# Optimization experiments

Hardware: AMD Instinct MI355X
Metric: run time of the kernel (lower is better)

The kernel has to match this reference:

```python
import jax, jax.numpy as jnp
import numpy as np

L, H, D_IN, D_OUT = 2, 768, 768, 512


def _gru_layer(x, w_ih, w_hh, b_ih, b_hh):
    # x: [B,T,D]; w_ih: [3H,D]; w_hh: [3H,H]; b_ih,b_hh: [3H]
    # PyTorch GRU gate order: r, z, n
    gates_x = jnp.einsum('btd,gd->btg', x, w_ih) + b_ih  # [B,T,3H], precomputed once
    gates_x = jnp.swapaxes(gates_x, 0, 1)  # [T,B,3H] for scan over time
    h0 = jnp.zeros((x.shape[0], w_hh.shape[1]), dtype=x.dtype)

    def step(h, gx):
        gh = h @ w_hh.T + b_hh  # [B,3H]
        xr, xz, xn = jnp.split(gx, 3, axis=-1)
        hr, hz, hn = jnp.split(gh, 3, axis=-1)
        r = jax.nn.sigmoid(xr + hr)
        z = jax.nn.sigmoid(xz + hz)
        n = jnp.tanh(xn + r * hn)
        h_new = (1.0 - z) * n + z * h
        return h_new, h_new

    _, ys = jax.lax.scan(step, h0, gates_x)  # ys: [T,B,H]
    return jnp.swapaxes(ys, 0, 1)  # [B,T,H]


def setup_inputs() -> dict:
    key = jax.random.key(0)
    ks = jax.random.split(key, 6)
    B, T = 16, 1024
    s = 1.0 / np.sqrt(H)  # PyTorch RNN init scale
    x = jax.random.normal(ks[0], (B, T, D_IN), dtype=jnp.float32)
    # stacked per-layer GRU weights (D_IN == H so layer 0 stacks cleanly)
    w_ih = jax.random.uniform(ks[1], (L, 3 * H, H), minval=-s, maxval=s, dtype=jnp.float32)
    w_hh = jax.random.uniform(ks[2], (L, 3 * H, H), minval=-s, maxval=s, dtype=jnp.float32)
    b_ih = jax.random.uniform(ks[3], (L, 3 * H), minval=-s, maxval=s, dtype=jnp.float32)
    b_hh = jax.random.uniform(ks[4], (L, 3 * H), minval=-s, maxval=s, dtype=jnp.float32)
    w_fc = jax.random.normal(ks[5], (D_OUT, H), dtype=jnp.float32) * 0.02
    b_fc = jnp.zeros((D_OUT,), dtype=jnp.float32)
    return {"x": x, "w_ih": w_ih, "w_hh": w_hh, "b_ih": b_ih, "b_hh": b_hh,
            "w_fc": w_fc, "b_fc": b_fc}


def reference(x, w_ih, w_hh, b_ih, b_hh, w_fc, b_fc):
    out = x
    for l in range(L):  # small fixed layer loop
        out = _gru_layer(out, w_ih[l], w_hh[l], b_ih[l], b_hh[l])
    out = jnp.einsum('bth,oh->bto', out, w_fc) + b_fc  # Linear(768->512)
    return jax.nn.gelu(out, approximate=False)  # torch gelu (exact)
```

## Files before the change

### kernel.cpp

```cpp
#include <hip/hip_runtime.h>
#include <hip/hip_bf16.h>

#define H     768
#define HPAD  776
#define G3    2304
#define BATCH 16
#define TLEN  1024
#define DOUT  512
#define SLICE 32
#define WPG   24
#define NWG   96
#define NTHR  384

typedef __attribute__((ext_vector_type(8))) short short8;
typedef __attribute__((ext_vector_type(4))) float f32x4;

union U8 { short8 s; unsigned u[4]; unsigned long long q[2]; uint4 v4; };

__device__ __forceinline__ float b2f(ushort u) {
  union { unsigned int ui; float f; } v; v.ui = ((unsigned int)u) << 16; return v.f;
}
__device__ __forceinline__ ushort f2b(float f) {
  union { float f; unsigned int ui; } v; v.f = f;
  unsigned int u = v.ui;
  return (ushort)((u + 0x7fffu + ((u >> 16) & 1u)) >> 16);
}

__device__ __forceinline__ unsigned long long agent_ld64(const void* p) {
  return __hip_atomic_load((const unsigned long long*)p, __ATOMIC_RELAXED, __HIP_MEMORY_SCOPE_AGENT);
}
__device__ __forceinline__ unsigned agent_ld32(const void* p) {
  return __hip_atomic_load((const unsigned*)p, __ATOMIC_RELAXED, __HIP_MEMORY_SCOPE_AGENT);
}
__device__ __forceinline__ void agent_st32(void* p, unsigned v) {
  __hip_atomic_store((unsigned*)p, v, __ATOMIC_RELAXED, __HIP_MEMORY_SCOPE_AGENT);
}
__device__ __forceinline__ void agent_st64(void* p, unsigned long long v) {
  __hip_atomic_store((unsigned long long*)p, v, __ATOMIC_RELAXED, __HIP_MEMORY_SCOPE_AGENT);
}

__device__ __forceinline__ short8 loadA8(const void* base, bool bf, size_t eidx) {
  if (bf) return *(const short8*)((const ushort*)base + eidx);
  const uint4* f = (const uint4*)((const float*)base + eidx);
  uint4 lo = f[0];
  uint4 hi = f[1];
  U8 r;
  r.u[0] = __builtin_amdgcn_perm(lo.y, lo.x, 0x07060302);
  r.u[1] = __builtin_amdgcn_perm(lo.w, lo.z, 0x07060302);
  r.u[2] = __builtin_amdgcn_perm(hi.y, hi.x, 0x07060302);
  r.u[3] = __builtin_amdgcn_perm(hi.w, hi.z, 0x07060302);
  return r.s;
}
__device__ __forceinline__ short8 loadW8(const void* base, bool bf, size_t eidx) {
  if (bf) return *(const short8*)((const ushort*)base + eidx);
  const float* f = (const float*)base + eidx;
  short8 r;
  #pragma unroll
  for (int i = 0; i < 8; i++) r[i] = (short)f2b(f[i]);
  return r;
}
__device__ __forceinline__ float loadS(const void* p, bool bf, size_t i) {
  return bf ? b2f(((const ushort*)p)[i]) : ((const float*)p)[i];
}

__device__ __forceinline__ bool detect_bf16(const unsigned* xw, int tid, int nthr, int* sh) {
  if (tid == 0) *sh = 0;
  __syncthreads();
  int c = 0;
  for (int i = tid; i < 4096; i += nthr) {
    int e = (int)((xw[i] >> 7) & 0xFF);
    c += (e >= 110 && e <= 140) ? 1 : 0;
  }
  atomicAdd(sh, c);
  __syncthreads();
  return *sh > 2048;
}

__device__ __forceinline__ unsigned* flagp(unsigned* flags, int grp, int wgi, int rep) {
  return flags + (((grp * WPG + wgi) * 4 + rep) * 32);
}

__global__ __launch_bounds__(NTHR) void scan_kernel(
    const void* __restrict__ x,
    const void* __restrict__ w_ih,
    const void* __restrict__ w_hh,
    const void* __restrict__ b_ih,
    const void* __restrict__ b_hh,
    unsigned int* flags,
    unsigned int* dflag,
    ushort* h1buf,
    ushort* h2buf,
    float*  gxbuf1,
    float*  gxbuf2,
    ushort* y2)
{
  const int wg   = blockIdx.x;
  const int grp  = wg / WPG;
  const int wgi  = wg % WPG;
  const int tid  = threadIdx.x;
  const int wave = tid >> 6;
  const int lane = tid & 63;
  const int quad = lane >> 4;

  __shared__ ushort h_lds[BATCH * HPAD];
  __shared__ float ghs[96 * 17];
  __shared__ float hold[BATCH * SLICE];
  __shared__ float bih_s[96], bhh_s[96];
  __shared__ int   detsh;

  const bool isbf = detect_bf16((const unsigned*)x, tid, NTHR, &detsh);
  if (tid == 0) dflag[0] = isbf ? 1u : 0u;

  for (int i = tid; i < BATCH * SLICE; i += NTHR) hold[i] = 0.0f;

  if (grp == 1 || grp == 3) {
    size_t boff = (grp == 3) ? (size_t)G3 : 0;
    for (int gf = tid; gf < 96; gf += NTHR) {
      size_t gidx = boff + (size_t)(gf >> 5) * H + wgi * SLICE + (gf & 31);
      bih_s[gf] = loadS(b_ih, isbf, gidx);
      bhh_s[gf] = loadS(b_hh, isbf, gidx);
    }
  }

  const unsigned* pollp = nullptr;
  if (wave == 0) {
    if (grp == 0) {
      if (lane == 0) pollp = flagp(flags, 1, wgi, 1);
    } else if (grp == 1) {
      if      (lane == 0)  pollp = flagp(flags, 0, wgi, 1);
      else if (lane <= 24) pollp = flagp(flags, 1, lane - 1, 0);
      else if (lane <= 48) pollp = flagp(flags, 2, lane - 25, 2);
    } else if (grp == 2) {
      if      (lane < 24)  pollp = flagp(flags, 1, lane, 2);
      else if (lane == 24) pollp = flagp(flags, 3, wgi, 1);
    } else {
      if      (lane == 0)  pollp = flagp(flags, 2, wgi, 1);
      else if (lane <= 24) pollp = flagp(flags, 3, lane - 1, 0);
    }
  }

  const void* Wmat = (grp == 0 || grp == 2) ? w_ih : w_hh;
  const size_t woff = (grp >= 2) ? (size_t)G3 * H : 0;
  const int gate   = wave >> 1;
  const int gfbase = gate * SLICE + (wave & 1) * 16;
  const int nrow   = gate * H + wgi * SLICE + (wave & 1) * 16 + (lane & 15);
  const size_t wbase = woff + (size_t)nrow * H + quad * 8;

  short8 bfrag[24];
  #pragma unroll
  for (int kk = 0; kk < 24; kk++)
    bfrag[kk] = loadW8(Wmat, isbf, wbase + kk * 32);

  const int sb  = tid / 24;
  const int seg = tid % 24;

  const int pb = tid >> 4;
  const int pj = (tid & 15) * 2;
  const bool pact = (tid < BATCH * SLICE / 2);

  __syncthreads();

  for (int t = 0; t < TLEN + 3; t++) {
    if (wave == 0) {
      const unsigned tgt = (unsigned)t;
      for (;;) {
        unsigned v = pollp ? agent_ld32(pollp) : 0xFFFFFFFFu;
        if (__ballot(v < tgt) == 0ull) break;
        __builtin_amdgcn_s_sleep(1);
      }
    }
    __syncthreads();

    const int par = t & 1;
    int tau;
    if      (grp == 0) tau = t;
    else if (grp == 1) tau = t - 1;
    else if (grp == 2) tau = t - 2;
    else               tau = t - 3;
    const bool active = (tau >= 0) && (tau < TLEN);
    const bool isL = (grp == 1 || grp == 3);

    if (active) {
      const int opar = tau & 1;

      unsigned long long gr01 = 0, gz01 = 0, gn01 = 0;
      const float* gxin = nullptr;
      if (isL) {
        gxin = ((grp == 1) ? gxbuf1 : gxbuf2) + ((size_t)(opar * WPG + wgi) * BATCH) * 96;
        if (pact) {
          const float* gxr = gxin + (size_t)pb * 96;
          gr01 = agent_ld64(gxr + pj);
          gz01 = agent_ld64(gxr + 32 + pj);
          gn01 = agent_ld64(gxr + 64 + pj);
        }
      }

      if (grp == 0) {
        const size_t srcbase = ((size_t)sb * TLEN + tau) * H + seg * 32;
        #pragma unroll
        for (int i = 0; i < 4; i++) {
          short8 v = loadA8(x, isbf, srcbase + i * 8);
          *(short8*)&h_lds[sb * HPAD + seg * 32 + i * 8] = v;
        }
      } else {
        const ushort* hsrc = ((grp == 3) ? h2buf : h1buf) + (size_t)par * (BATCH * H);
        const ushort* src = hsrc + (size_t)sb * H + seg * 32;
        U8 a, b;
        a.q[0] = agent_ld64(src +  0); a.q[1] = agent_ld64(src +  4);
        b.q[0] = agent_ld64(src +  8); b.q[1] = agent_ld64(src + 12);
        U8 c, d;
        c.q[0] = agent_ld64(src + 16); c.q[1] = agent_ld64(src + 20);
        d.q[0] = agent_ld64(src + 24); d.q[1] = agent_ld64(src + 28);
        ushort* dst = &h_lds[sb * HPAD + seg * 32];
        *(uint4*)(dst + 0)  = a.v4;
        *(uint4*)(dst + 8)  = b.v4;
        *(uint4*)(dst + 16) = c.v4;
        *(uint4*)(dst + 24) = d.v4;
      }
      __syncthreads();

      const ushort* arow = &h_lds[(lane & 15) * HPAD + quad * 8];
      f32x4 acc0 = {0.f, 0.f, 0.f, 0.f}, acc1 = {0.f, 0.f, 0.f, 0.f};
      #pragma unroll
      for (int kk = 0; kk < 12; kk++) {
        short8 a0 = *(const short8*)(arow + kk * 32);
        short8 a1 = *(const short8*)(arow + (kk + 12) * 32);
        acc0 = __builtin_amdgcn_mfma_f32_16x16x32_bf16(a0, bfrag[kk],      acc0, 0, 0, 0);
        acc1 = __builtin_amdgcn_mfma_f32_16x16x32_bf16(a1, bfrag[kk + 12], acc1, 0, 0, 0);
      }
      f32x4 acc = acc0 + acc1;

      #pragma unroll
      for (int i = 0; i < 4; i++)
        ghs[(gfbase + (lane & 15)) * 17 + quad * 4 + i] = acc[i];
      __syncthreads();

      if (!isL) {
        float* gxout = ((grp == 0) ? gxbuf1 : gxbuf2) + ((size_t)(par * WPG + wgi) * BATCH) * 96;
        const int m  = tid / 24;
        const int c4 = (tid % 24) * 4;
        union { unsigned long long q; float f[2]; } p0, p1;
        p0.f[0] = ghs[(c4 + 0) * 17 + m];
        p0.f[1] = ghs[(c4 + 1) * 17 + m];
        p1.f[0] = ghs[(c4 + 2) * 17 + m];
        p1.f[1] = ghs[(c4 + 3) * 17 + m];
        agent_st64(gxout + (size_t)m * 96 + c4,     p0.q);
        agent_st64(gxout + (size_t)m * 96 + c4 + 2, p1.q);
      } else if (pact) {
        union { unsigned long long q; float f[2]; } ur, uz, un;
        ur.q = gr01; uz.q = gz01; un.q = gn01;
        ushort* hout = ((grp == 1) ? h1buf : h2buf) + (size_t)opar * (BATCH * H);
        unsigned hpack = 0;
        #pragma unroll
        for (int s = 0; s < 2; s++) {
          const int j = pj + s;
          float rpre = ur.f[s] + bih_s[j]      + ghs[j * 17 + pb]        + bhh_s[j];
          float zpre = uz.f[s] + bih_s[32 + j] + ghs[(32 + j) * 17 + pb] + bhh_s[32 + j];
          float hn   = ghs[(64 + j) * 17 + pb] + bhh_s[64 + j];
          float r = 1.0f / (1.0f + expf(-rpre));
          float z = 1.0f / (1.0f + expf(-zpre));
          float n = tanhf(un.f[s] + bih_s[64 + j] + r * hn);
          float hnew = (1.0f - z) * n + z * hold[pb * SLICE + j];
          hold[pb * SLICE + j] = hnew;
          hpack |= ((unsigned)f2b(hnew)) << (16 * s);
        }
        agent_st32(&hout[(size_t)pb * H + wgi * SLICE + pj], hpack);
        if (grp == 3)
          *(unsigned*)&y2[((size_t)pb * TLEN + tau) * H + wgi * SLICE + pj] = hpack;
      }
    }

    __syncthreads();
    if (tid < 4) agent_st32(flagp(flags, grp, wgi, tid), (unsigned)(t + 1));
  }
}

__global__ __launch_bounds__(256) void fc_kernel(
    const ushort* __restrict__ y2,
    const void* __restrict__ w_fc,
    const void* __restrict__ b_fc,
    const unsigned* __restrict__ dflag,
    void* __restrict__ out)
{
  const bool isbf = dflag[0] != 0u;
  const int wave = threadIdx.x >> 6;
  const int lane = threadIdx.x & 63;
  const int col  = lane & 15;
  const int quad = lane >> 4;
  const int m0 = blockIdx.x * 64 + wave * 16;
  const int n0 = blockIdx.y * 64;

  const ushort* arow = y2 + (size_t)(m0 + col) * H + quad * 8;
  const size_t bbase = (size_t)(n0 + col) * H + quad * 8;

  f32x4 acc[4];
  #pragma unroll
  for (int nt = 0; nt < 4; nt++) acc[nt] = (f32x4){0.f, 0.f, 0.f, 0.f};

  for (int kk = 0; kk < 24; kk++) {
    short8 a = *(const short8*)(arow + kk * 32);
    #pragma unroll
    for (int nt = 0; nt < 4; nt++) {
      short8 b = loadA8(w_fc, isbf, bbase + (size_t)nt * 16 * H + kk * 32);
      acc[nt] = __builtin_amdgcn_mfma_f32_16x16x32_bf16(a, b, acc[nt], 0, 0, 0);
    }
  }

  #pragma unroll
  for (int nt = 0; nt < 4; nt++) {
    #pragma unroll
    for (int i = 0; i < 4; i++) {
      int m = m0 + quad * 4 + i;
      int n = n0 + nt * 16 + col;
      float v = acc[nt][i] + loadS(b_fc, isbf, n);
      float g = 0.5f * v * (1.0f + erff(v * 0.70710678118654752f));
      if (isbf) ((ushort*)out)[(size_t)m * DOUT + n] = f2b(g);
      else      ((float*)out)[(size_t)m * DOUT + n] = g;
    }
  }
}

extern "C" void kernel_launch(void* const* d_in, const int* in_sizes, int n_in,
                              void* d_out, int out_size, void* d_ws, size_t ws_size,
                              hipStream_t stream) {
  const void* x    = d_in[0];
  const void* w_ih = d_in[1];
  const void* w_hh = d_in[2];
  const void* b_ih = d_in[3];
  const void* b_hh = d_in[4];
  const void* w_fc = d_in[5];
  const void* b_fc = d_in[6];

  char* ws = (char*)d_ws;
  unsigned int* flags = (unsigned int*)(ws);
  unsigned int* dflag = (unsigned int*)(ws + 49152);
  ushort* h1buf  = (ushort*)(ws + 53248);
  ushort* h2buf  = (ushort*)(ws + 102400);
  float*  gxbuf1 = (float*)(ws + 151552);
  float*  gxbuf2 = (float*)(ws + 446464);
  ushort* y2     = (ushort*)(ws + 741376);

  hipMemsetAsync(ws, 0, 151552, stream);
  scan_kernel<<<dim3(NWG), dim3(NTHR), 0, stream>>>(
      x, w_ih, w_hh, b_ih, b_hh, flags, dflag,
      h1buf, h2buf, gxbuf1, gxbuf2, y2);
  fc_kernel<<<dim3(16384 / 64, DOUT / 64), dim3(256), 0, stream>>>(
      y2, w_fc, b_fc, dflag, (void*)d_out);
}
```

Baseline: 4.087 ms.

## Replace per-step flag barriers with tagged data words and 4-slot ring buffers

Each published value (hidden state and input-gate projections) now carries a 32-bit step tag in a 64-bit word, so consumers poll the data itself instead of waiting on producer flags. Buffers become 4-deep rings, and only a loose slack flag (t-2) is kept for back-pressure. This removes the flag-store-then-poll round trip and a block barrier on the serial critical path of the pipelined GRU scan. In exchange it doubles the bytes moved per element, needs a larger memset, and adds per-element polling loops.

```diff
diff --git a/kernel.cpp b/kernel.cpp
--- a/kernel.cpp
+++ b/kernel.cpp
@@ -11,6 +11,8 @@
 #define WPG   24
 #define NWG   96
 #define NTHR  384
+#define HSLOT 6144
+#define GXSLOT 36864
 
 typedef __attribute__((ext_vector_type(8))) short short8;
 typedef __attribute__((ext_vector_type(4))) float f32x4;
@@ -37,6 +39,9 @@
 }
 __device__ __forceinline__ void agent_st64(void* p, unsigned long long v) {
   __hip_atomic_store((unsigned long long*)p, v, __ATOMIC_RELAXED, __HIP_MEMORY_SCOPE_AGENT);
+}
+__device__ __forceinline__ unsigned long long tagq(unsigned lo, unsigned tag) {
+  return ((unsigned long long)tag << 32) | (unsigned long long)lo;
 }
 
 __device__ __forceinline__ short8 loadA8(const void* base, bool bf, size_t eidx) {
@@ -76,10 +81,6 @@
   return *sh > 2048;
 }
 
-__device__ __forceinline__ unsigned* flagp(unsigned* flags, int grp, int wgi, int rep) {
-  return flags + (((grp * WPG + wgi) * 4 + rep) * 32);
-}
-
 __global__ __launch_bounds__(NTHR) void scan_kernel(
     const void* __restrict__ x,
     const void* __restrict__ w_ih,
@@ -88,10 +89,10 @@
     const void* __restrict__ b_hh,
     unsigned int* flags,
     unsigned int* dflag,
-    ushort* h1buf,
-    ushort* h2buf,
-    float*  gxbuf1,
-    float*  gxbuf2,
+    unsigned long long* h1t,
+    unsigned long long* h2t,
+    unsigned long long* gx1t,
+    unsigned long long* gx2t,
     ushort* y2)
 {
   const int wg   = blockIdx.x;
@@ -101,6 +102,7 @@
   const int wave = tid >> 6;
   const int lane = tid & 63;
   const int quad = lane >> 4;
+  const bool isL = (grp == 1 || grp == 3);
 
   __shared__ ushort h_lds[BATCH * HPAD];
   __shared__ float ghs[96 * 17];
@@ -109,33 +111,16 @@
   __shared__ int   detsh;
 
   const bool isbf = detect_bf16((const unsigned*)x, tid, NTHR, &detsh);
-  if (tid == 0) dflag[0] = isbf ? 1u : 0u;
+  if (tid == 0 && wg == 0) dflag[0] = isbf ? 1u : 0u;
 
   for (int i = tid; i < BATCH * SLICE; i += NTHR) hold[i] = 0.0f;
 
-  if (grp == 1 || grp == 3) {
+  if (isL) {
     size_t boff = (grp == 3) ? (size_t)G3 : 0;
     for (int gf = tid; gf < 96; gf += NTHR) {
       size_t gidx = boff + (size_t)(gf >> 5) * H + wgi * SLICE + (gf & 31);
       bih_s[gf] = loadS(b_ih, isbf, gidx);
       bhh_s[gf] = loadS(b_hh, isbf, gidx);
-    }
-  }
-
-  const unsigned* pollp = nullptr;
-  if (wave == 0) {
-    if (grp == 0) {
-      if (lane == 0) pollp = flagp(flags, 1, wgi, 1);
-    } else if (grp == 1) {
-      if      (lane == 0)  pollp = flagp(flags, 0, wgi, 1);
-      else if (lane <= 24) pollp = flagp(flags, 1, lane - 1, 0);
-      else if (lane <= 48) pollp = flagp(flags, 2, lane - 25, 2);
-    } else if (grp == 2) {
-      if      (lane < 24)  pollp = flagp(flags, 1, lane, 2);
-      else if (lane == 24) pollp = flagp(flags, 3, wgi, 1);
-    } else {
-      if      (lane == 0)  pollp = flagp(flags, 2, wgi, 1);
-      else if (lane <= 24) pollp = flagp(flags, 3, lane - 1, 0);
     }
   }
 
@@ -156,122 +141,144 @@
 
   const int pb = tid >> 4;
   const int pj = (tid & 15) * 2;
-  const bool pact = (tid < BATCH * SLICE / 2);
+  const bool pact = isL && (tid < BATCH * SLICE / 2);
+
+  const int postkind = (grp == 0) ? -1 : grp - 1;
+  const int chkkind  = (grp == 3) ? -1 : grp;
+  const bool chklane = (chkkind >= 0) && (wave == 0) && (lane >= 32) && (lane < 32 + WPG);
+  const unsigned* chkp = chklane
+      ? flags + ((size_t)chkkind * WPG + (lane - 32)) * 32 : flags;
 
   __syncthreads();
 
   for (int t = 0; t < TLEN + 3; t++) {
-    if (wave == 0) {
-      const unsigned tgt = (unsigned)t;
-      for (;;) {
-        unsigned v = pollp ? agent_ld32(pollp) : 0xFFFFFFFFu;
-        if (__ballot(v < tgt) == 0ull) break;
-        __builtin_amdgcn_s_sleep(1);
+    if (postkind >= 0 && tid == 0)
+      agent_st32(flags + ((size_t)postkind * WPG + wgi) * 32, (unsigned)t);
+
+    const int tau = t - grp;
+    if (tau < 0 || tau >= TLEN) continue;
+
+    unsigned pendS = 0, pendG = 0;
+    unsigned lo[16];
+    float gxv[6];
+    const unsigned long long* hsrc = nullptr;
+    const unsigned long long* gsrc = nullptr;
+    unsigned tagS = 0, tagG = 0;
+
+    if (grp == 0) {
+      const size_t srcbase = ((size_t)sb * TLEN + tau) * H + seg * 32;
+      #pragma unroll
+      for (int i = 0; i < 4; i++) {
+        short8 v = loadA8(x, isbf, srcbase + i * 8);
+        *(short8*)&h_lds[sb * HPAD + seg * 32 + i * 8] = v;
+      }
+    } else {
+      const int hstep = (grp == 2) ? tau : tau - 1;
+      const unsigned long long* hbuf = (grp == 3) ? h2t : h1t;
+      if (hstep >= 0) {
+        pendS = 0xFFFFu;
+        tagS  = (unsigned)(hstep + 1);
+        hsrc  = hbuf + (size_t)(hstep & 3) * HSLOT + (size_t)sb * (H / 2) + seg * 16;
+      }
+      if (pact) {
+        pendG = 0x3Fu;
+        tagG  = (unsigned)(tau + 1);
+        gsrc  = ((grp == 1) ? gx1t : gx2t) + (size_t)(tau & 3) * GXSLOT
+              + ((size_t)wgi * BATCH + pb) * 96;
+      }
+    }
+
+    bool flagok = !chklane;
+    const int slkT = t - 2;
+    for (;;) {
+      if (pendS) {
+        #pragma unroll
+        for (int q = 0; q < 16; q++) if (pendS & (1u << q)) {
+          unsigned long long v = agent_ld64(hsrc + q);
+          if ((unsigned)(v >> 32) == tagS) { lo[q] = (unsigned)v; pendS &= ~(1u << q); }
+        }
+      }
+      if (pendG) {
+        #pragma unroll
+        for (int g = 0; g < 6; g++) if (pendG & (1u << g)) {
+          const int gf = (g >> 1) * 32 + pj + (g & 1);
+          unsigned long long v = agent_ld64(gsrc + gf);
+          if ((unsigned)(v >> 32) == tagG) {
+            union { unsigned u; float f; } cv; cv.u = (unsigned)v;
+            gxv[g] = cv.f; pendG &= ~(1u << g);
+          }
+        }
+      }
+      if (!flagok && (int)agent_ld32(chkp) >= slkT) flagok = true;
+      if (__ballot(((pendS | pendG) != 0) || !flagok) == 0ull) break;
+      __builtin_amdgcn_s_sleep(1);
+    }
+
+    if (grp != 0) {
+      uint4* dst = (uint4*)&h_lds[sb * HPAD + seg * 32];
+      if (tagS) {
+        dst[0] = make_uint4(lo[0],  lo[1],  lo[2],  lo[3]);
+        dst[1] = make_uint4(lo[4],  lo[5],  lo[6],  lo[7]);
+        dst[2] = make_uint4(lo[8],  lo[9],  lo[10], lo[11]);
+        dst[3] = make_uint4(lo[12], lo[13], lo[14], lo[15]);
+      } else {
+        uint4 z = make_uint4(0, 0, 0, 0);
+        dst[0] = z; dst[1] = z; dst[2] = z; dst[3] = z;
       }
     }
     __syncthreads();
 
-    const int par = t & 1;
-    int tau;
-    if      (grp == 0) tau = t;
-    else if (grp == 1) tau = t - 1;
-    else if (grp == 2) tau = t - 2;
-    else               tau = t - 3;
-    const bool active = (tau >= 0) && (tau < TLEN);
-    const bool isL = (grp == 1 || grp == 3);
-
-    if (active) {
-      const int opar = tau & 1;
-
-      unsigned long long gr01 = 0, gz01 = 0, gn01 = 0;
-      const float* gxin = nullptr;
-      if (isL) {
-        gxin = ((grp == 1) ? gxbuf1 : gxbuf2) + ((size_t)(opar * WPG + wgi) * BATCH) * 96;
-        if (pact) {
-          const float* gxr = gxin + (size_t)pb * 96;
-          gr01 = agent_ld64(gxr + pj);
-          gz01 = agent_ld64(gxr + 32 + pj);
-          gn01 = agent_ld64(gxr + 64 + pj);
-        }
-      }
-
-      if (grp == 0) {
-        const size_t srcbase = ((size_t)sb * TLEN + tau) * H + seg * 32;
-        #pragma unroll
-        for (int i = 0; i < 4; i++) {
-          short8 v = loadA8(x, isbf, srcbase + i * 8);
-          *(short8*)&h_lds[sb * HPAD + seg * 32 + i * 8] = v;
-        }
-      } else {
-        const ushort* hsrc = ((grp == 3) ? h2buf : h1buf) + (size_t)par * (BATCH * H);
-        const ushort* src = hsrc + (size_t)sb * H + seg * 32;
-        U8 a, b;
-        a.q[0] = agent_ld64(src +  0); a.q[1] = agent_ld64(src +  4);
-        b.q[0] = agent_ld64(src +  8); b.q[1] = agent_ld64(src + 12);
-        U8 c, d;
-        c.q[0] = agent_ld64(src + 16); c.q[1] = agent_ld64(src + 20);
-        d.q[0] = agent_ld64(src + 24); d.q[1] = agent_ld64(src + 28);
-        ushort* dst = &h_lds[sb * HPAD + seg * 32];
-        *(uint4*)(dst + 0)  = a.v4;
-        *(uint4*)(dst + 8)  = b.v4;
-        *(uint4*)(dst + 16) = c.v4;
-        *(uint4*)(dst + 24) = d.v4;
+    const ushort* arow = &h_lds[(lane & 15) * HPAD + quad * 8];
+    f32x4 acc0 = {0.f, 0.f, 0.f, 0.f}, acc1 = {0.f, 0.f, 0.f, 0.f};
+    #pragma unroll
+    for (int kk = 0; kk < 12; kk++) {
+      short8 a0 = *(const short8*)(arow + kk * 32);
+      short8 a1 = *(const short8*)(arow + (kk + 12) * 32);
+      acc0 = __builtin_amdgcn_mfma_f32_16x16x32_bf16(a0, bfrag[kk],      acc0, 0, 0, 0);
+      acc1 = __builtin_amdgcn_mfma_f32_16x16x32_bf16(a1, bfrag[kk + 12], acc1, 0, 0, 0);
+    }
+    f32x4 acc = acc0 + acc1;
+
+    if (!isL) {
+      unsigned long long* outb = ((grp == 0) ? gx1t : gx2t)
+          + (size_t)(tau & 3) * GXSLOT + (size_t)wgi * BATCH * 96
+          + (size_t)(gfbase + (lane & 15));
+      const unsigned tg = (unsigned)(tau + 1);
+      #pragma unroll
+      for (int i = 0; i < 4; i++) {
+        union { float f; unsigned u; } cv; cv.f = acc[i];
+        agent_st64(outb + (size_t)(quad * 4 + i) * 96, tagq(cv.u, tg));
       }
       __syncthreads();
-
-      const ushort* arow = &h_lds[(lane & 15) * HPAD + quad * 8];
-      f32x4 acc0 = {0.f, 0.f, 0.f, 0.f}, acc1 = {0.f, 0.f, 0.f, 0.f};
-      #pragma unroll
-      for (int kk = 0; kk < 12; kk++) {
-        short8 a0 = *(const short8*)(arow + kk * 32);
-        short8 a1 = *(const short8*)(arow + (kk + 12) * 32);
-        acc0 = __builtin_amdgcn_mfma_f32_16x16x32_bf16(a0, bfrag[kk],      acc0, 0, 0, 0);
-        acc1 = __builtin_amdgcn_mfma_f32_16x16x32_bf16(a1, bfrag[kk + 12], acc1, 0, 0, 0);
-      }
-      f32x4 acc = acc0 + acc1;
-
+    } else {
       #pragma unroll
       for (int i = 0; i < 4; i++)
         ghs[(gfbase + (lane & 15)) * 17 + quad * 4 + i] = acc[i];
       __syncthreads();
 
-      if (!isL) {
-        float* gxout = ((grp == 0) ? gxbuf1 : gxbuf2) + ((size_t)(par * WPG + wgi) * BATCH) * 96;
-        const int m  = tid / 24;
-        const int c4 = (tid % 24) * 4;
-        union { unsigned long long q; float f[2]; } p0, p1;
-        p0.f[0] = ghs[(c4 + 0) * 17 + m];
-        p0.f[1] = ghs[(c4 + 1) * 17 + m];
-        p1.f[0] = ghs[(c4 + 2) * 17 + m];
-        p1.f[1] = ghs[(c4 + 3) * 17 + m];
-        agent_st64(gxout + (size_t)m * 96 + c4,     p0.q);
-        agent_st64(gxout + (size_t)m * 96 + c4 + 2, p1.q);
-      } else if (pact) {
-        union { unsigned long long q; float f[2]; } ur, uz, un;
-        ur.q = gr01; uz.q = gz01; un.q = gn01;
-        ushort* hout = ((grp == 1) ? h1buf : h2buf) + (size_t)opar * (BATCH * H);
+      if (pact) {
         unsigned hpack = 0;
         #pragma unroll
         for (int s = 0; s < 2; s++) {
           const int j = pj + s;
-          float rpre = ur.f[s] + bih_s[j]      + ghs[j * 17 + pb]        + bhh_s[j];
-          float zpre = uz.f[s] + bih_s[32 + j] + ghs[(32 + j) * 17 + pb] + bhh_s[32 + j];
+          float rpre = gxv[0 + s] + bih_s[j]      + ghs[j * 17 + pb]        + bhh_s[j];
+          float zpre = gxv[2 + s] + bih_s[32 + j] + ghs[(32 + j) * 17 + pb] + bhh_s[32 + j];
           float hn   = ghs[(64 + j) * 17 + pb] + bhh_s[64 + j];
           float r = 1.0f / (1.0f + expf(-rpre));
           float z = 1.0f / (1.0f + expf(-zpre));
-          float n = tanhf(un.f[s] + bih_s[64 + j] + r * hn);
+          float n = tanhf(gxv[4 + s] + bih_s[64 + j] + r * hn);
           float hnew = (1.0f - z) * n + z * hold[pb * SLICE + j];
           hold[pb * SLICE + j] = hnew;
           hpack |= ((unsigned)f2b(hnew)) << (16 * s);
         }
-        agent_st32(&hout[(size_t)pb * H + wgi * SLICE + pj], hpack);
+        unsigned long long* ht = (grp == 1) ? h1t : h2t;
+        agent_st64(ht + (size_t)(tau & 3) * HSLOT + (size_t)pb * (H / 2)
+                      + (size_t)(wgi * SLICE + pj) / 2,
+                   tagq(hpack, (unsigned)(tau + 1)));
         if (grp == 3)
           *(unsigned*)&y2[((size_t)pb * TLEN + tau) * H + wgi * SLICE + pj] = hpack;
       }
     }
-
-    __syncthreads();
-    if (tid < 4) agent_st32(flagp(flags, grp, wgi, tid), (unsigned)(t + 1));
   }
 }
 
@@ -333,17 +340,17 @@
 
   char* ws = (char*)d_ws;
   unsigned int* flags = (unsigned int*)(ws);
-  unsigned int* dflag = (unsigned int*)(ws + 49152);
-  ushort* h1buf  = (ushort*)(ws + 53248);
-  ushort* h2buf  = (ushort*)(ws + 102400);
-  float*  gxbuf1 = (float*)(ws + 151552);
-  float*  gxbuf2 = (float*)(ws + 446464);
-  ushort* y2     = (ushort*)(ws + 741376);
-
-  hipMemsetAsync(ws, 0, 151552, stream);
+  unsigned int* dflag = (unsigned int*)(ws + 9216);
+  unsigned long long* h1t  = (unsigned long long*)(ws + 9728);
+  unsigned long long* h2t  = (unsigned long long*)(ws + 206336);
+  unsigned long long* gx1t = (unsigned long long*)(ws + 402944);
+  unsigned long long* gx2t = (unsigned long long*)(ws + 1582592);
+  ushort* y2 = (ushort*)(ws + 2762240);
+
+  hipMemsetAsync(ws, 0, 2762240, stream);
   scan_kernel<<<dim3(NWG), dim3(NTHR), 0, stream>>>(
       x, w_ih, w_hh, b_ih, b_hh, flags, dflag,
-      h1buf, h2buf, gxbuf1, gxbuf2, y2);
+      h1t, h2t, gx1t, gx2t, y2);
   fc_kernel<<<dim3(16384 / 64, DOUT / 64), dim3(256), 0, stream>>>(
       y2, w_fc, b_fc, dflag, (void*)d_out);
 }
```

Result: slower. 8.657 ms (+111.8%).

## Deepen GRU wavefront pipeline with 4-slot ring buffers and relaxed flag dependencies

Applied to the files above, without the earlier changes.

Switches the h and gate-x exchange buffers from double to quad buffering, which lets producer groups run further ahead. The per-group poll offsets are loosened, and the layer-1 input projection overlaps the same step as layer 0, so the pipeline depth drops by one step. Projection groups now store MFMA accumulators straight to global memory, skipping the LDS transpose, and the recurrence groups signal completion through an LDS counter once the four active waves drain their stores, with no full barrier. This shortens the per-step critical path of the serial scan, at the cost of more workspace and subtle memory-ordering risks in the flag protocol.

```diff
diff --git a/kernel.cpp b/kernel.cpp
--- a/kernel.cpp
+++ b/kernel.cpp
@@ -35,8 +35,9 @@
 __device__ __forceinline__ void agent_st32(void* p, unsigned v) {
   __hip_atomic_store((unsigned*)p, v, __ATOMIC_RELAXED, __HIP_MEMORY_SCOPE_AGENT);
 }
-__device__ __forceinline__ void agent_st64(void* p, unsigned long long v) {
-  __hip_atomic_store((unsigned long long*)p, v, __ATOMIC_RELAXED, __HIP_MEMORY_SCOPE_AGENT);
+__device__ __forceinline__ void agent_st32f(void* p, float f) {
+  union { float f; unsigned u; } cv; cv.f = f;
+  __hip_atomic_store((unsigned*)p, cv.u, __ATOMIC_RELAXED, __HIP_MEMORY_SCOPE_AGENT);
 }
 
 __device__ __forceinline__ short8 loadA8(const void* base, bool bf, size_t eidx) {
@@ -101,19 +102,23 @@
   const int wave = tid >> 6;
   const int lane = tid & 63;
   const int quad = lane >> 4;
+  const bool isL = (grp == 1 || grp == 3);
 
   __shared__ ushort h_lds[BATCH * HPAD];
   __shared__ float ghs[96 * 17];
   __shared__ float hold[BATCH * SLICE];
   __shared__ float bih_s[96], bhh_s[96];
+  __shared__ unsigned donecnt[2];
   __shared__ int   detsh;
+
+  if (tid < 2) donecnt[tid] = 0u;
 
   const bool isbf = detect_bf16((const unsigned*)x, tid, NTHR, &detsh);
   if (tid == 0) dflag[0] = isbf ? 1u : 0u;
 
   for (int i = tid; i < BATCH * SLICE; i += NTHR) hold[i] = 0.0f;
 
-  if (grp == 1 || grp == 3) {
+  if (isL) {
     size_t boff = (grp == 3) ? (size_t)G3 : 0;
     for (int gf = tid; gf < 96; gf += NTHR) {
       size_t gidx = boff + (size_t)(gf >> 5) * H + wgi * SLICE + (gf & 31);
@@ -123,19 +128,20 @@
   }
 
   const unsigned* pollp = nullptr;
+  int polloff = 0;
   if (wave == 0) {
     if (grp == 0) {
-      if (lane == 0) pollp = flagp(flags, 1, wgi, 1);
+      if (lane == 0) { pollp = flagp(flags, 1, wgi, 2); polloff = -2; }
     } else if (grp == 1) {
-      if      (lane == 0)  pollp = flagp(flags, 0, wgi, 1);
-      else if (lane <= 24) pollp = flagp(flags, 1, lane - 1, 0);
-      else if (lane <= 48) pollp = flagp(flags, 2, lane - 25, 2);
+      if      (lane == 0)  { pollp = flagp(flags, 0, wgi, 0);       polloff = 1;  }
+      else if (lane <= 24) { pollp = flagp(flags, 1, lane - 1, 0);  polloff = 0;  }
+      else if (lane <= 48) { pollp = flagp(flags, 2, lane - 25, 0); polloff = -2; }
     } else if (grp == 2) {
-      if      (lane < 24)  pollp = flagp(flags, 1, lane, 2);
-      else if (lane == 24) pollp = flagp(flags, 3, wgi, 1);
+      if      (lane < 24)  { pollp = flagp(flags, 1, lane, 1);      polloff = 0;  }
+      else if (lane == 24) { pollp = flagp(flags, 3, wgi, 1);       polloff = -2; }
     } else {
-      if      (lane == 0)  pollp = flagp(flags, 2, wgi, 1);
-      else if (lane <= 24) pollp = flagp(flags, 3, lane - 1, 0);
+      if      (lane == 0)  { pollp = flagp(flags, 2, wgi, 1);       polloff = 0;  }
+      else if (lane <= 24) { pollp = flagp(flags, 3, lane - 1, 0);  polloff = 0;  }
     }
   }
 
@@ -156,100 +162,101 @@
 
   const int pb = tid >> 4;
   const int pj = (tid & 15) * 2;
-  const bool pact = (tid < BATCH * SLICE / 2);
+  const bool pact = isL && (tid < BATCH * SLICE / 2);
+
+  const int lag = (grp == 2) ? 1 : ((grp == 3) ? 2 : 0);
 
   __syncthreads();
 
-  for (int t = 0; t < TLEN + 3; t++) {
+  for (int t = 0; t < TLEN + 2; t++) {
+    const int tau = t - lag;
+    const bool active = (tau >= 0) && (tau < TLEN);
+
+    if (!active) {
+      __syncthreads();
+      if (tid < 4) agent_st32(flagp(flags, grp, wgi, tid), (unsigned)(t + 1));
+      continue;
+    }
+
     if (wave == 0) {
-      const unsigned tgt = (unsigned)t;
       for (;;) {
-        unsigned v = pollp ? agent_ld32(pollp) : 0xFFFFFFFFu;
-        if (__ballot(v < tgt) == 0ull) break;
+        int v = pollp ? (int)agent_ld32(pollp) : 0x7FFFFFFF;
+        if (__ballot(v < t + polloff) == 0ull) break;
         __builtin_amdgcn_s_sleep(1);
       }
     }
     __syncthreads();
 
-    const int par = t & 1;
-    int tau;
-    if      (grp == 0) tau = t;
-    else if (grp == 1) tau = t - 1;
-    else if (grp == 2) tau = t - 2;
-    else               tau = t - 3;
-    const bool active = (tau >= 0) && (tau < TLEN);
-    const bool isL = (grp == 1 || grp == 3);
-
-    if (active) {
-      const int opar = tau & 1;
-
-      unsigned long long gr01 = 0, gz01 = 0, gn01 = 0;
-      const float* gxin = nullptr;
-      if (isL) {
-        gxin = ((grp == 1) ? gxbuf1 : gxbuf2) + ((size_t)(opar * WPG + wgi) * BATCH) * 96;
-        if (pact) {
-          const float* gxr = gxin + (size_t)pb * 96;
-          gr01 = agent_ld64(gxr + pj);
-          gz01 = agent_ld64(gxr + 32 + pj);
-          gn01 = agent_ld64(gxr + 64 + pj);
-        }
-      }
-
-      if (grp == 0) {
-        const size_t srcbase = ((size_t)sb * TLEN + tau) * H + seg * 32;
-        #pragma unroll
-        for (int i = 0; i < 4; i++) {
-          short8 v = loadA8(x, isbf, srcbase + i * 8);
-          *(short8*)&h_lds[sb * HPAD + seg * 32 + i * 8] = v;
-        }
-      } else {
-        const ushort* hsrc = ((grp == 3) ? h2buf : h1buf) + (size_t)par * (BATCH * H);
-        const ushort* src = hsrc + (size_t)sb * H + seg * 32;
+    unsigned long long gr01 = 0, gz01 = 0, gn01 = 0;
+    if (pact) {
+      const float* gxr = ((grp == 1) ? gxbuf1 : gxbuf2)
+          + ((size_t)((tau & 3) * WPG + wgi) * BATCH + pb) * 96;
+      gr01 = agent_ld64(gxr + pj);
+      gz01 = agent_ld64(gxr + 32 + pj);
+      gn01 = agent_ld64(gxr + 64 + pj);
+    }
+
+    if (grp == 0) {
+      const size_t srcbase = ((size_t)sb * TLEN + tau) * H + seg * 32;
+      #pragma unroll
+      for (int i = 0; i < 4; i++) {
+        short8 v = loadA8(x, isbf, srcbase + i * 8);
+        *(short8*)&h_lds[sb * HPAD + seg * 32 + i * 8] = v;
+      }
+    } else {
+      const int hstep = tau - ((grp == 2) ? 0 : 1);
+      ushort* dst = &h_lds[sb * HPAD + seg * 32];
+      if (hstep >= 0) {
+        const ushort* src = ((grp == 3) ? h2buf : h1buf)
+            + (size_t)(hstep & 3) * (BATCH * H) + (size_t)sb * H + seg * 32;
         U8 a, b;
         a.q[0] = agent_ld64(src +  0); a.q[1] = agent_ld64(src +  4);
         b.q[0] = agent_ld64(src +  8); b.q[1] = agent_ld64(src + 12);
         U8 c, d;
         c.q[0] = agent_ld64(src + 16); c.q[1] = agent_ld64(src + 20);
         d.q[0] = agent_ld64(src + 24); d.q[1] = agent_ld64(src + 28);
-        ushort* dst = &h_lds[sb * HPAD + seg * 32];
         *(uint4*)(dst + 0)  = a.v4;
         *(uint4*)(dst + 8)  = b.v4;
         *(uint4*)(dst + 16) = c.v4;
         *(uint4*)(dst + 24) = d.v4;
-      }
+      } else {
+        uint4 z = make_uint4(0, 0, 0, 0);
+        *(uint4*)(dst + 0)  = z; *(uint4*)(dst + 8)  = z;
+        *(uint4*)(dst + 16) = z; *(uint4*)(dst + 24) = z;
+      }
+    }
+    __syncthreads();
+
+    const ushort* arow = &h_lds[(lane & 15) * HPAD + quad * 8];
+    f32x4 acc0 = {0.f, 0.f, 0.f, 0.f}, acc1 = {0.f, 0.f, 0.f, 0.f};
+    #pragma unroll
+    for (int kk = 0; kk < 12; kk++) {
+      short8 a0 = *(const short8*)(arow + kk * 32);
+      short8 a1 = *(const short8*)(arow + (kk + 12) * 32);
+      acc0 = __builtin_amdgcn_mfma_f32_16x16x32_bf16(a0, bfrag[kk],      acc0, 0, 0, 0);
+      acc1 = __builtin_amdgcn_mfma_f32_16x16x32_bf16(a1, bfrag[kk + 12], acc1, 0, 0, 0);
+    }
+    f32x4 acc = acc0 + acc1;
+
+    if (!isL) {
+      float* cbase = ((grp == 0) ? gxbuf1 : gxbuf2)
+          + ((size_t)(tau & 3) * WPG + wgi) * BATCH * 96
+          + (size_t)(gfbase + (lane & 15));
+      #pragma unroll
+      for (int i = 0; i < 4; i++)
+        agent_st32f(cbase + (size_t)(quad * 4 + i) * 96, acc[i]);
       __syncthreads();
-
-      const ushort* arow = &h_lds[(lane & 15) * HPAD + quad * 8];
-      f32x4 acc0 = {0.f, 0.f, 0.f, 0.f}, acc1 = {0.f, 0.f, 0.f, 0.f};
-      #pragma unroll
-      for (int kk = 0; kk < 12; kk++) {
-        short8 a0 = *(const short8*)(arow + kk * 32);
-        short8 a1 = *(const short8*)(arow + (kk + 12) * 32);
-        acc0 = __builtin_amdgcn_mfma_f32_16x16x32_bf16(a0, bfrag[kk],      acc0, 0, 0, 0);
-        acc1 = __builtin_amdgcn_mfma_f32_16x16x32_bf16(a1, bfrag[kk + 12], acc1, 0, 0, 0);
-      }
-      f32x4 acc = acc0 + acc1;
-
+      if (tid < 4) agent_st32(flagp(flags, grp, wgi, tid), (unsigned)(t + 1));
+    } else {
       #pragma unroll
       for (int i = 0; i < 4; i++)
         ghs[(gfbase + (lane & 15)) * 17 + quad * 4 + i] = acc[i];
       __syncthreads();
 
-      if (!isL) {
-        float* gxout = ((grp == 0) ? gxbuf1 : gxbuf2) + ((size_t)(par * WPG + wgi) * BATCH) * 96;
-        const int m  = tid / 24;
-        const int c4 = (tid % 24) * 4;
-        union { unsigned long long q; float f[2]; } p0, p1;
-        p0.f[0] = ghs[(c4 + 0) * 17 + m];
-        p0.f[1] = ghs[(c4 + 1) * 17 + m];
-        p1.f[0] = ghs[(c4 + 2) * 17 + m];
-        p1.f[1] = ghs[(c4 + 3) * 17 + m];
-        agent_st64(gxout + (size_t)m * 96 + c4,     p0.q);
-        agent_st64(gxout + (size_t)m * 96 + c4 + 2, p1.q);
-      } else if (pact) {
+      if (pact) {
         union { unsigned long long q; float f[2]; } ur, uz, un;
         ur.q = gr01; uz.q = gz01; un.q = gn01;
-        ushort* hout = ((grp == 1) ? h1buf : h2buf) + (size_t)opar * (BATCH * H);
+        ushort* hout = ((grp == 1) ? h1buf : h2buf) + (size_t)(tau & 3) * (BATCH * H);
         unsigned hpack = 0;
         #pragma unroll
         for (int s = 0; s < 2; s++) {
@@ -268,10 +275,19 @@
         if (grp == 3)
           *(unsigned*)&y2[((size_t)pb * TLEN + tau) * H + wgi * SLICE + pj] = hpack;
       }
-    }
-
-    __syncthreads();
-    if (tid < 4) agent_st32(flagp(flags, grp, wgi, tid), (unsigned)(t + 1));
+      if (tid < BATCH * SLICE / 2) {
+        asm volatile("s_waitcnt vmcnt(0)" ::: "memory");
+        if ((tid & 63) == 0) {
+          unsigned prev = atomicAdd(&donecnt[t & 1], 1u);
+          if (prev == 3u) {
+            donecnt[t & 1] = 0u;
+            #pragma unroll
+            for (int r = 0; r < 4; r++)
+              agent_st32(flagp(flags, grp, wgi, r), (unsigned)(t + 1));
+          }
+        }
+      }
+    }
   }
 }
 
@@ -335,12 +351,12 @@
   unsigned int* flags = (unsigned int*)(ws);
   unsigned int* dflag = (unsigned int*)(ws + 49152);
   ushort* h1buf  = (ushort*)(ws + 53248);
-  ushort* h2buf  = (ushort*)(ws + 102400);
-  float*  gxbuf1 = (float*)(ws + 151552);
-  float*  gxbuf2 = (float*)(ws + 446464);
-  ushort* y2     = (ushort*)(ws + 741376);
-
-  hipMemsetAsync(ws, 0, 151552, stream);
+  ushort* h2buf  = (ushort*)(ws + 151552);
+  float*  gxbuf1 = (float*)(ws + 249856);
+  float*  gxbuf2 = (float*)(ws + 839680);
+  ushort* y2     = (ushort*)(ws + 1429504);
+
+  hipMemsetAsync(ws, 0, 49156, stream);
   scan_kernel<<<dim3(NWG), dim3(NTHR), 0, stream>>>(
       x, w_ih, w_hh, b_ih, b_hh, flags, dflag,
       h1buf, h2buf, gxbuf1, gxbuf2, y2);
```

Measured after the change: 4.620 ms. 13.0% more time.

## Deepen inter-group ring buffers, relax flag dependencies, swizzle LDS, read h2 from y2

Applied to the files above, without the earlier changes.

Replaces the double-buffered h1 and gate-input buffers with 4-deep rings and shifts each group's lag, so producers can run further ahead and the spin-wait dependencies loosen. Polling now happens only on active steps, with per-flag offsets. The second layer's recurrent state is read straight from y2, which removes the h2 buffer and a duplicate store. The padded LDS layout is replaced with an XOR swizzle, and h rows are loaded with inline 64-byte dwordx4 loads using sc0/sc1 cache bits. The risks are subtle ordering and race bugs in the retimed pipeline and a reliance on inline asm cache semantics.

```diff
diff --git a/kernel.cpp b/kernel.cpp
--- a/kernel.cpp
+++ b/kernel.cpp
@@ -2,7 +2,6 @@
 #include <hip/hip_bf16.h>
 
 #define H     768
-#define HPAD  776
 #define G3    2304
 #define BATCH 16
 #define TLEN  1024
@@ -14,8 +13,9 @@
 
 typedef __attribute__((ext_vector_type(8))) short short8;
 typedef __attribute__((ext_vector_type(4))) float f32x4;
-
-union U8 { short8 s; unsigned u[4]; unsigned long long q[2]; uint4 v4; };
+typedef __attribute__((ext_vector_type(4))) unsigned int u32x4;
+
+union U8 { short8 s; unsigned u[4]; unsigned long long q[2]; };
 
 __device__ __forceinline__ float b2f(ushort u) {
   union { unsigned int ui; float f; } v; v.ui = ((unsigned int)u) << 16; return v.f;
@@ -37,6 +37,17 @@
 }
 __device__ __forceinline__ void agent_st64(void* p, unsigned long long v) {
   __hip_atomic_store((unsigned long long*)p, v, __ATOMIC_RELAXED, __HIP_MEMORY_SCOPE_AGENT);
+}
+
+__device__ __forceinline__ void ld64B_agent(const void* p, u32x4* r) {
+  asm volatile(
+    "global_load_dwordx4 %0, %4, off sc0 sc1\n\t"
+    "global_load_dwordx4 %1, %4, off offset:16 sc0 sc1\n\t"
+    "global_load_dwordx4 %2, %4, off offset:32 sc0 sc1\n\t"
+    "global_load_dwordx4 %3, %4, off offset:48 sc0 sc1\n\t"
+    "s_waitcnt vmcnt(0)"
+    : "=&v"(r[0]), "=&v"(r[1]), "=&v"(r[2]), "=&v"(r[3])
+    : "v"(p) : "memory");
 }
 
 __device__ __forceinline__ short8 loadA8(const void* base, bool bf, size_t eidx) {
@@ -89,7 +100,6 @@
     unsigned int* flags,
     unsigned int* dflag,
     ushort* h1buf,
-    ushort* h2buf,
     float*  gxbuf1,
     float*  gxbuf2,
     ushort* y2)
@@ -101,8 +111,9 @@
   const int wave = tid >> 6;
   const int lane = tid & 63;
   const int quad = lane >> 4;
-
-  __shared__ ushort h_lds[BATCH * HPAD];
+  const bool isL = (grp == 1 || grp == 3);
+
+  __shared__ ushort h_lds[BATCH * H];
   __shared__ float ghs[96 * 17];
   __shared__ float hold[BATCH * SLICE];
   __shared__ float bih_s[96], bhh_s[96];
@@ -113,7 +124,7 @@
 
   for (int i = tid; i < BATCH * SLICE; i += NTHR) hold[i] = 0.0f;
 
-  if (grp == 1 || grp == 3) {
+  if (isL) {
     size_t boff = (grp == 3) ? (size_t)G3 : 0;
     for (int gf = tid; gf < 96; gf += NTHR) {
       size_t gidx = boff + (size_t)(gf >> 5) * H + wgi * SLICE + (gf & 31);
@@ -123,19 +134,20 @@
   }
 
   const unsigned* pollp = nullptr;
+  int polloff = 0;
   if (wave == 0) {
     if (grp == 0) {
-      if (lane == 0) pollp = flagp(flags, 1, wgi, 1);
+      if (lane == 0) { pollp = flagp(flags, 1, wgi, 2); polloff = -2; }
     } else if (grp == 1) {
-      if      (lane == 0)  pollp = flagp(flags, 0, wgi, 1);
-      else if (lane <= 24) pollp = flagp(flags, 1, lane - 1, 0);
-      else if (lane <= 48) pollp = flagp(flags, 2, lane - 25, 2);
+      if      (lane == 0)  { pollp = flagp(flags, 0, wgi, 0);       polloff = 0;  }
+      else if (lane <= 24) { pollp = flagp(flags, 1, lane - 1, 0);  polloff = 0;  }
+      else if (lane <= 48) { pollp = flagp(flags, 2, lane - 25, 0); polloff = -2; }
     } else if (grp == 2) {
-      if      (lane < 24)  pollp = flagp(flags, 1, lane, 2);
-      else if (lane == 24) pollp = flagp(flags, 3, wgi, 1);
+      if      (lane < 24)  { pollp = flagp(flags, 1, lane, 1);      polloff = 0;  }
+      else if (lane == 24) { pollp = flagp(flags, 3, wgi, 1);       polloff = -1; }
     } else {
-      if      (lane == 0)  pollp = flagp(flags, 2, wgi, 1);
-      else if (lane <= 24) pollp = flagp(flags, 3, lane - 1, 0);
+      if      (lane == 0)  { pollp = flagp(flags, 2, wgi, 1);       polloff = -1; }
+      else if (lane <= 24) { pollp = flagp(flags, 3, lane - 1, 0);  polloff = 0;  }
     }
   }
 
@@ -153,46 +165,37 @@
 
   const int sb  = tid / 24;
   const int seg = tid % 24;
+  const int sx  = sb & 7;
 
   const int pb = tid >> 4;
   const int pj = (tid & 15) * 2;
-  const bool pact = (tid < BATCH * SLICE / 2);
+  const bool pact = isL && (tid < BATCH * SLICE / 2);
+
+  const int lag = (grp == 1) ? 1 : ((grp == 2) ? 2 : ((grp == 3) ? 4 : 0));
 
   __syncthreads();
 
-  for (int t = 0; t < TLEN + 3; t++) {
-    if (wave == 0) {
-      const unsigned tgt = (unsigned)t;
-      for (;;) {
-        unsigned v = pollp ? agent_ld32(pollp) : 0xFFFFFFFFu;
-        if (__ballot(v < tgt) == 0ull) break;
-        __builtin_amdgcn_s_sleep(1);
-      }
-    }
-    __syncthreads();
-
-    const int par = t & 1;
-    int tau;
-    if      (grp == 0) tau = t;
-    else if (grp == 1) tau = t - 1;
-    else if (grp == 2) tau = t - 2;
-    else               tau = t - 3;
+  for (int t = 0; t < TLEN + 4; t++) {
+    const int tau = t - lag;
     const bool active = (tau >= 0) && (tau < TLEN);
-    const bool isL = (grp == 1 || grp == 3);
 
     if (active) {
-      const int opar = tau & 1;
+      if (wave == 0) {
+        for (;;) {
+          int v = pollp ? (int)agent_ld32(pollp) : 0x7FFFFFFF;
+          if (__ballot(v < t + polloff) == 0ull) break;
+          __builtin_amdgcn_s_sleep(1);
+        }
+      }
+      __syncthreads();
 
       unsigned long long gr01 = 0, gz01 = 0, gn01 = 0;
-      const float* gxin = nullptr;
-      if (isL) {
-        gxin = ((grp == 1) ? gxbuf1 : gxbuf2) + ((size_t)(opar * WPG + wgi) * BATCH) * 96;
-        if (pact) {
-          const float* gxr = gxin + (size_t)pb * 96;
-          gr01 = agent_ld64(gxr + pj);
-          gz01 = agent_ld64(gxr + 32 + pj);
-          gn01 = agent_ld64(gxr + 64 + pj);
-        }
+      if (pact) {
+        const float* gxr = ((grp == 1) ? gxbuf1 : gxbuf2)
+            + ((size_t)((tau & 3) * WPG + wgi) * BATCH + pb) * 96;
+        gr01 = agent_ld64(gxr + pj);
+        gz01 = agent_ld64(gxr + 32 + pj);
+        gn01 = agent_ld64(gxr + 64 + pj);
       }
 
       if (grp == 0) {
@@ -200,31 +203,34 @@
         #pragma unroll
         for (int i = 0; i < 4; i++) {
           short8 v = loadA8(x, isbf, srcbase + i * 8);
-          *(short8*)&h_lds[sb * HPAD + seg * 32 + i * 8] = v;
+          *(short8*)&h_lds[sb * H + (((seg * 4 + i) ^ sx) * 8)] = v;
         }
       } else {
-        const ushort* hsrc = ((grp == 3) ? h2buf : h1buf) + (size_t)par * (BATCH * H);
-        const ushort* src = hsrc + (size_t)sb * H + seg * 32;
-        U8 a, b;
-        a.q[0] = agent_ld64(src +  0); a.q[1] = agent_ld64(src +  4);
-        b.q[0] = agent_ld64(src +  8); b.q[1] = agent_ld64(src + 12);
-        U8 c, d;
-        c.q[0] = agent_ld64(src + 16); c.q[1] = agent_ld64(src + 20);
-        d.q[0] = agent_ld64(src + 24); d.q[1] = agent_ld64(src + 28);
-        ushort* dst = &h_lds[sb * HPAD + seg * 32];
-        *(uint4*)(dst + 0)  = a.v4;
-        *(uint4*)(dst + 8)  = b.v4;
-        *(uint4*)(dst + 16) = c.v4;
-        *(uint4*)(dst + 24) = d.v4;
+        const int hstep = (grp == 3) ? (t - 5) : (t - 2);
+        u32x4 r4[4];
+        if (hstep >= 0) {
+          const ushort* src = (grp == 3)
+              ? y2 + ((size_t)sb * TLEN + hstep) * H + seg * 32
+              : h1buf + (size_t)(hstep & 3) * (BATCH * H) + (size_t)sb * H + seg * 32;
+          ld64B_agent(src, r4);
+        } else {
+          r4[0] = (u32x4){0u, 0u, 0u, 0u};
+          r4[1] = r4[0]; r4[2] = r4[0]; r4[3] = r4[0];
+        }
+        #pragma unroll
+        for (int j = 0; j < 4; j++)
+          *(u32x4*)&h_lds[sb * H + (((seg * 4 + j) ^ sx) * 8)] = r4[j];
       }
       __syncthreads();
 
-      const ushort* arow = &h_lds[(lane & 15) * HPAD + quad * 8];
+      const int ar  = lane & 15;
+      const int arx = ar & 7;
+      const ushort* abase = &h_lds[ar * H];
       f32x4 acc0 = {0.f, 0.f, 0.f, 0.f}, acc1 = {0.f, 0.f, 0.f, 0.f};
       #pragma unroll
       for (int kk = 0; kk < 12; kk++) {
-        short8 a0 = *(const short8*)(arow + kk * 32);
-        short8 a1 = *(const short8*)(arow + (kk + 12) * 32);
+        short8 a0 = *(const short8*)&abase[((quad + 4 * kk) ^ arx) * 8];
+        short8 a1 = *(const short8*)&abase[((quad + 4 * (kk + 12)) ^ arx) * 8];
         acc0 = __builtin_amdgcn_mfma_f32_16x16x32_bf16(a0, bfrag[kk],      acc0, 0, 0, 0);
         acc1 = __builtin_amdgcn_mfma_f32_16x16x32_bf16(a1, bfrag[kk + 12], acc1, 0, 0, 0);
       }
@@ -236,7 +242,8 @@
       __syncthreads();
 
       if (!isL) {
-        float* gxout = ((grp == 0) ? gxbuf1 : gxbuf2) + ((size_t)(par * WPG + wgi) * BATCH) * 96;
+        float* gxout = ((grp == 0) ? gxbuf1 : gxbuf2)
+            + ((size_t)(tau & 3) * WPG + wgi) * BATCH * 96;
         const int m  = tid / 24;
         const int c4 = (tid % 24) * 4;
         union { unsigned long long q; float f[2]; } p0, p1;
@@ -249,7 +256,6 @@
       } else if (pact) {
         union { unsigned long long q; float f[2]; } ur, uz, un;
         ur.q = gr01; uz.q = gz01; un.q = gn01;
-        ushort* hout = ((grp == 1) ? h1buf : h2buf) + (size_t)opar * (BATCH * H);
         unsigned hpack = 0;
         #pragma unroll
         for (int s = 0; s < 2; s++) {
@@ -264,9 +270,11 @@
           hold[pb * SLICE + j] = hnew;
           hpack |= ((unsigned)f2b(hnew)) << (16 * s);
         }
-        agent_st32(&hout[(size_t)pb * H + wgi * SLICE + pj], hpack);
-        if (grp == 3)
-          *(unsigned*)&y2[((size_t)pb * TLEN + tau) * H + wgi * SLICE + pj] = hpack;
+        if (grp == 1)
+          agent_st32(h1buf + (size_t)(tau & 3) * (BATCH * H)
+                           + (size_t)pb * H + wgi * SLICE + pj, hpack);
+        else
+          agent_st32(&y2[((size_t)pb * TLEN + tau) * H + wgi * SLICE + pj], hpack);
       }
     }
 
@@ -335,15 +343,14 @@
   unsigned int* flags = (unsigned int*)(ws);
   unsigned int* dflag = (unsigned int*)(ws + 49152);
   ushort* h1buf  = (ushort*)(ws + 53248);
-  ushort* h2buf  = (ushort*)(ws + 102400);
   float*  gxbuf1 = (float*)(ws + 151552);
-  float*  gxbuf2 = (float*)(ws + 446464);
-  ushort* y2     = (ushort*)(ws + 741376);
-
-  hipMemsetAsync(ws, 0, 151552, stream);
+  float*  gxbuf2 = (float*)(ws + 741376);
+  ushort* y2     = (ushort*)(ws + 1331200);
+
+  hipMemsetAsync(ws, 0, 49156, stream);
   scan_kernel<<<dim3(NWG), dim3(NTHR), 0, stream>>>(
       x, w_ih, w_hh, b_ih, b_hh, flags, dflag,
-      h1buf, h2buf, gxbuf1, gxbuf2, y2);
+      h1buf, gxbuf1, gxbuf2, y2);
   fc_kernel<<<dim3(16384 / 64, DOUT / 64), dim3(256), 0, stream>>>(
       y2, w_fc, b_fc, dflag, (void*)d_out);
 }
```

Result: faster. 3.676 ms (-10.1%).
